# Performance work log

Hardware: AMD Instinct MI355X
Metric: run time of the kernel (lower is better)

The kernel has to match this reference:

```python
import jax, jax.numpy as jnp
import numpy as np

K = 8        # fused SOS sections
C = 64       # channels (B*C after reshape)
T = 262144   # time samples (~6 s @ 44.1 kHz)


def setup_inputs() -> dict:
    key = jax.random.key(0)
    kx, kb, ka1, ka2 = jax.random.split(key, 4)
    x = jax.random.normal(kx, (C, T), dtype=jnp.float32)
    # Stable biquad coefficients: a0 = 1, |a1| < 0.5, |a2| < 0.4 keeps poles
    # strictly inside the unit circle (|a1| < 1 + a2 and |a2| < 1).
    b = jax.random.normal(kb, (K, 3), dtype=jnp.float32) * 0.3
    a1 = jax.random.uniform(ka1, (K, 1), minval=-0.5, maxval=0.5, dtype=jnp.float32)
    a2 = jax.random.uniform(ka2, (K, 1), minval=-0.4, maxval=0.4, dtype=jnp.float32)
    sos = jnp.concatenate([b, jnp.ones((K, 1), jnp.float32), a1, a2], axis=1)
    state_x = jnp.zeros((K, C, 2), jnp.float32)  # [x[n-1], x[n-2]] per section/channel
    state_y = jnp.zeros((K, C, 2), jnp.float32)  # [y[n-1], y[n-2]]
    return {"x": x, "sos": sos, "state_x": state_x, "state_y": state_y}


def _biquad_df1(x, b0, b1, b2, a1, a2, sx, sy):
    """Direct-form-1 biquad over time, vectorized across channels.

    x: [C, T]; sx, sy: [C, 2] holding (lag1, lag2). Returns y: [C, T].
    """
    def step(carry, xn):
        x1, x2, y1, y2 = carry
        yn = b0 * xn + b1 * x1 + b2 * x2 - a1 * y1 - a2 * y2
        return (xn, x1, yn, y1), yn

    init = (sx[:, 0], sx[:, 1], sy[:, 0], sy[:, 1])
    _, ys = jax.lax.scan(step, init, x.T)  # scan over T, carry [C]
    return ys.T


def reference(x, sos, state_x, state_y):
    # Serial cascade of K second-order sections (fallback path of forward()).
    out = x
    k = sos.shape[0]
    for s in range(k):
        out = _biquad_df1(out, sos[s, 0], sos[s, 1], sos[s, 2],
                          sos[s, 4], sos[s, 5], state_x[s], state_y[s])
    return out
```

## Files before the change

### kernel.cpp

```cpp
#include <hip/hip_runtime.h>

#define C 64
#define T 262144
#define K 8
#define KH 4
#define L 256
#define W 192
#define B (T / L)
#define TT 64
#define STRIDE 65
#define TMAX (T - 16)

#define STEP4(Y1, Y2, U1, U2, XIN)                                           \
  {                                                                          \
    float tkv[KH];                                                           \
    tkv[0] = fmaf(b1c[0], U1,                                                \
             fmaf(b2c[0], U2, fmaf(na1[0], Y1[0], na2[0] * Y2[0])));         \
    _Pragma("unroll")                                                        \
    for (int k = 1; k < KH; ++k)                                             \
      tkv[k] = fmaf(b1c[k], Y1[k - 1],                                       \
               fmaf(b2c[k], Y2[k - 1],                                       \
               fmaf(na1[k], Y1[k], na2[k] * Y2[k])));                        \
    float o = fmaf(b0c[0], (XIN), tkv[0]);                                   \
    U2 = (XIN);                                                              \
    _Pragma("unroll")                                                        \
    for (int k = 1; k < KH; ++k) {                                           \
      float o2 = fmaf(b0c[k], o, tkv[k]);                                    \
      Y2[k - 1] = o;                                                         \
      o = o2;                                                                \
    }                                                                        \
    Y2[KH - 1] = o;                                                          \
    lastout = o;                                                             \
  }

#define GROUP_W0(XS, ROW, CB)                                                \
  _Pragma("unroll")                                                          \
  for (int jj = 0; jj < 16; jj += 2) {                                       \
    STEP4(yA, yB, uA, uB, XS[jj])                                            \
    (ROW)[(CB) + jj] = lastout;                                              \
    STEP4(yB, yA, uB, uA, XS[jj + 1])                                        \
    (ROW)[(CB) + jj + 1] = lastout;                                          \
  }

#define LOAD16(DST, PTR)                                                     \
  {                                                                          \
    const float4* p4_ = (const float4*)(PTR);                                \
    float4 q0_ = p4_[0], q1_ = p4_[1], q2_ = p4_[2], q3_ = p4_[3];           \
    DST[0] = q0_.x;  DST[1] = q0_.y;  DST[2] = q0_.z;  DST[3] = q0_.w;       \
    DST[4] = q1_.x;  DST[5] = q1_.y;  DST[6] = q1_.z;  DST[7] = q1_.w;       \
    DST[8] = q2_.x;  DST[9] = q2_.y;  DST[10] = q2_.z; DST[11] = q2_.w;      \
    DST[12] = q3_.x; DST[13] = q3_.y; DST[14] = q3_.z; DST[15] = q3_.w;      \
  }

__global__ __launch_bounds__(128) void sos_kernel(
    const float* __restrict__ x, const float* __restrict__ sos,
    const float* __restrict__ sx, const float* __restrict__ sy,
    float* __restrict__ out) {
  __shared__ float hbuf[2][64 * STRIDE];

  const int h = blockIdx.x;
  const int b = (h & 7) * (B / 8) + (h >> 3);
  const int wid = threadIdx.x >> 6;
  const int lane = threadIdx.x & 63;

  float b0c[KH], b1c[KH], b2c[KH], na1[KH], na2[KH];
#pragma unroll
  for (int k = 0; k < KH; ++k) {
    const int kg = wid * KH + k;
    b0c[k] = sos[kg * 6 + 0];
    b1c[k] = sos[kg * 6 + 1];
    b2c[k] = sos[kg * 6 + 2];
    na1[k] = -sos[kg * 6 + 4];
    na2[k] = -sos[kg * 6 + 5];
  }

  const int t_out = b * L;
  const int tstart = (t_out >= W) ? (t_out - W) : 0;
  const int nwarm = (t_out - tstart) / TT;
  const int nch = nwarm + L / TT;

  const float* xrow = x + (size_t)lane * T;

  float yA[KH], yB[KH], uA, uB;
  if (tstart == 0) {
    uA = sx[(wid * 256 + lane) * 2 + 0];
    uB = sx[(wid * 256 + lane) * 2 + 1];
#pragma unroll
    for (int k = 0; k < KH; ++k) {
      const int kg = wid * KH + k;
      yA[k] = sy[(kg * 64 + lane) * 2 + 0];
      yB[k] = sy[(kg * 64 + lane) * 2 + 1];
    }
  } else {
    if (wid == 0) {
      uA = xrow[tstart - 1];
      uB = xrow[tstart - 2];
    } else {
      uA = 0.f;
      uB = 0.f;
    }
#pragma unroll
    for (int k = 0; k < KH; ++k) { yA[k] = 0.f; yB[k] = 0.f; }
  }

  float xA[16], xB[16], xC[16], xD[16];
  if (wid == 0) {
    LOAD16(xA, xrow + tstart)
    LOAD16(xB, xrow + tstart + 16)
  }

  float lastout = 0.f;
  for (int p = 0; p <= nch; ++p) {
    if (wid == 0) {
      if (p < nch) {
        const int tc = tstart + p * TT;
        float* myrow = &hbuf[p & 1][lane * STRIDE];
        LOAD16(xC, xrow + tc + 32)
        GROUP_W0(xA, myrow, 0)
        LOAD16(xD, xrow + tc + 48)
        GROUP_W0(xB, myrow, 16)
        { int tl = tc + 64;  if (tl > TMAX) tl = TMAX;
          LOAD16(xA, xrow + tl) }
        GROUP_W0(xC, myrow, 32)
        { int tl = tc + 80;  if (tl > TMAX) tl = TMAX;
          LOAD16(xB, xrow + tl) }
        GROUP_W0(xD, myrow, 48)
      }
    } else {
      const int q = p - 1;
      if (q >= 0) {
        const int tq = tstart + q * TT;
        float* myrow = &hbuf[q & 1][lane * STRIDE];
        float xg0[8], xg1[8];
#pragma unroll
        for (int j = 0; j < 8; ++j) xg0[j] = myrow[j];
        for (int gg = 0; gg < 4; ++gg) {
          const int tb = gg * 16;
#pragma unroll
          for (int j = 0; j < 8; ++j) xg1[j] = myrow[tb + 8 + j];
#pragma unroll
          for (int j = 0; j < 8; j += 2) {
            STEP4(yA, yB, uA, uB, xg0[j])
            myrow[tb + j] = lastout;
            STEP4(yB, yA, uB, uA, xg0[j + 1])
            myrow[tb + j + 1] = lastout;
          }
          if (gg + 1 < 4) {
#pragma unroll
            for (int j = 0; j < 8; ++j) xg0[j] = myrow[tb + 16 + j];
          }
#pragma unroll
          for (int j = 0; j < 8; j += 2) {
            STEP4(yA, yB, uA, uB, xg1[j])
            myrow[tb + 8 + j] = lastout;
            STEP4(yB, yA, uB, uA, xg1[j + 1])
            myrow[tb + 8 + j + 1] = lastout;
          }
        }
        if (q >= nwarm) {
          const float* lbuf = hbuf[q & 1];
          const int rr = lane >> 4;
          const int cc = (lane & 15) * 4;
#pragma unroll
          for (int it = 0; it < 16; ++it) {
            const int r = it * 4 + rr;
            float4 v;
            v.x = lbuf[r * STRIDE + cc + 0];
            v.y = lbuf[r * STRIDE + cc + 1];
            v.z = lbuf[r * STRIDE + cc + 2];
            v.w = lbuf[r * STRIDE + cc + 3];
            *reinterpret_cast<float4*>(&out[(size_t)r * T + tq + cc]) = v;
          }
        }
      }
    }
    __syncthreads();
  }
  (void)lastout;
}

extern "C" void kernel_launch(void* const* d_in, const int* in_sizes, int n_in,
                              void* d_out, int out_size, void* d_ws,
                              size_t ws_size, hipStream_t stream) {
  const float* x = (const float*)d_in[0];
  const float* sos = (const float*)d_in[1];
  const float* sx = (const float*)d_in[2];
  const float* sy = (const float*)d_in[3];
  float* out = (float*)d_out;
  (void)d_ws;

  sos_kernel<<<B, 128, 0, stream>>>(x, sos, sx, sy, out);
}
```

Before: 134.9 us.

## Write second-stage outputs directly to global and use lighter barrier

The second wave no longer writes its filtered results back to shared memory and then re-reads them for a transposed coalesced store. It now stores float4 chunks straight from registers into each lane's own output row, and skips the stores entirely during warm-up chunks. The __syncthreads is replaced by an LDS-only waitcnt plus s_barrier, so global stores no longer stall at the barrier. The trade-off is that each lane writes a separate row, so global stores become strided across lanes rather than coalesced.

New measurement: 141.8 us. 5.1% more time.

```diff
diff --git a/kernel.cpp b/kernel.cpp
--- a/kernel.cpp
+++ b/kernel.cpp
@@ -10,6 +10,12 @@
 #define TT 64
 #define STRIDE 65
 #define TMAX (T - 16)
+
+__device__ __forceinline__ void phase_barrier() {
+  __asm__ __volatile__("s_waitcnt lgkmcnt(0)" ::: "memory");
+  __builtin_amdgcn_s_barrier();
+  __asm__ __volatile__("" ::: "memory");
+}
 
 #define STEP4(Y1, Y2, U1, U2, XIN)                                           \
   {                                                                          \
@@ -41,6 +47,28 @@
     STEP4(yB, yA, uB, uA, XS[jj + 1])                                        \
     (ROW)[(CB) + jj + 1] = lastout;                                          \
   }
+
+#define GROUP_W1_OUT(XS, CB)                                                 \
+  _Pragma("unroll")                                                          \
+  for (int jj = 0; jj < 16; jj += 4) {                                       \
+    float4 ov_;                                                              \
+    STEP4(yA, yB, uA, uB, XS[jj])     ov_.x = lastout;                       \
+    STEP4(yB, yA, uB, uA, XS[jj + 1]) ov_.y = lastout;                       \
+    STEP4(yA, yB, uA, uB, XS[jj + 2]) ov_.z = lastout;                       \
+    STEP4(yB, yA, uB, uA, XS[jj + 3]) ov_.w = lastout;                       \
+    *reinterpret_cast<float4*>(&outrow[(CB) + jj]) = ov_;                    \
+  }
+
+#define GROUP_W1_WARM(XS)                                                    \
+  _Pragma("unroll")                                                          \
+  for (int jj = 0; jj < 16; jj += 2) {                                       \
+    STEP4(yA, yB, uA, uB, XS[jj])                                            \
+    STEP4(yB, yA, uB, uA, XS[jj + 1])                                        \
+  }
+
+#define RD16(DST, OFF)                                                       \
+  _Pragma("unroll")                                                          \
+  for (int j = 0; j < 16; ++j) DST[j] = myrow[(OFF) + j];
 
 #define LOAD16(DST, PTR)                                                     \
   {                                                                          \
@@ -130,51 +158,29 @@
       const int q = p - 1;
       if (q >= 0) {
         const int tq = tstart + q * TT;
-        float* myrow = &hbuf[q & 1][lane * STRIDE];
-        float xg0[8], xg1[8];
-#pragma unroll
-        for (int j = 0; j < 8; ++j) xg0[j] = myrow[j];
-        for (int gg = 0; gg < 4; ++gg) {
-          const int tb = gg * 16;
-#pragma unroll
-          for (int j = 0; j < 8; ++j) xg1[j] = myrow[tb + 8 + j];
-#pragma unroll
-          for (int j = 0; j < 8; j += 2) {
-            STEP4(yA, yB, uA, uB, xg0[j])
-            myrow[tb + j] = lastout;
-            STEP4(yB, yA, uB, uA, xg0[j + 1])
-            myrow[tb + j + 1] = lastout;
-          }
-          if (gg + 1 < 4) {
-#pragma unroll
-            for (int j = 0; j < 8; ++j) xg0[j] = myrow[tb + 16 + j];
-          }
-#pragma unroll
-          for (int j = 0; j < 8; j += 2) {
-            STEP4(yA, yB, uA, uB, xg1[j])
-            myrow[tb + 8 + j] = lastout;
-            STEP4(yB, yA, uB, uA, xg1[j + 1])
-            myrow[tb + 8 + j + 1] = lastout;
-          }
-        }
+        const float* myrow = &hbuf[q & 1][lane * STRIDE];
+        float xg0[16], xg1[16];
+        RD16(xg0, 0)
+        RD16(xg1, 16)
         if (q >= nwarm) {
-          const float* lbuf = hbuf[q & 1];
-          const int rr = lane >> 4;
-          const int cc = (lane & 15) * 4;
-#pragma unroll
-          for (int it = 0; it < 16; ++it) {
-            const int r = it * 4 + rr;
-            float4 v;
-            v.x = lbuf[r * STRIDE + cc + 0];
-            v.y = lbuf[r * STRIDE + cc + 1];
-            v.z = lbuf[r * STRIDE + cc + 2];
-            v.w = lbuf[r * STRIDE + cc + 3];
-            *reinterpret_cast<float4*>(&out[(size_t)r * T + tq + cc]) = v;
-          }
+          float* outrow = out + (size_t)lane * T + tq;
+          GROUP_W1_OUT(xg0, 0)
+          RD16(xg0, 32)
+          GROUP_W1_OUT(xg1, 16)
+          RD16(xg1, 48)
+          GROUP_W1_OUT(xg0, 32)
+          GROUP_W1_OUT(xg1, 48)
+        } else {
+          GROUP_W1_WARM(xg0)
+          RD16(xg0, 32)
+          GROUP_W1_WARM(xg1)
+          RD16(xg1, 48)
+          GROUP_W1_WARM(xg0)
+          GROUP_W1_WARM(xg1)
         }
       }
     }
-    __syncthreads();
+    phase_barrier();
   }
   (void)lastout;
 }
```
